# Optimization experiments

Measured on AMD Instinct MI355X. Metric: run time of the kernel, lower is better.

The kernel has to match this reference:

```python
import jax, jax.numpy as jnp
import numpy as np

N, M, D = 16384, 1024, 1024


def setup_inputs() -> dict:
    key = jax.random.key(0)
    kq, kp = jax.random.split(key)
    query = jax.random.normal(kq, (N, D), dtype=jnp.float32)
    proto = jax.random.normal(kp, (M, D), dtype=jnp.float32)
    return {"query": query, "proto": proto}


def reference(query, proto):
    # Pairwise squared euclidean: ||q||^2 - 2 q.p + ||p||^2  (same math as
    # the expand+pow+sum in compute_euclidean, but without the [N,M,D] blowup).
    q2 = jnp.sum(query * query, axis=-1, keepdims=True)          # [N,1]
    p2 = jnp.sum(proto * proto, axis=-1)                          # [M]
    qp = jnp.einsum('nd,md->nm', query, proto)                    # [N,M]
    dists = q2 - 2.0 * qp + p2[None, :]                           # [N,M]
    # Original applies F.softmax(-dists, dim=1) (named log_p_y but is softmax).
    return jax.nn.softmax(-dists, axis=1)
```

## Files before the change

### kernel.cpp

```cpp
#include <hip/hip_runtime.h>
#include <stdint.h>

#define N_Q 16384
#define M_P 1024
#define D_K 1024

typedef __attribute__((ext_vector_type(8))) __bf16 bf16x8;
typedef __attribute__((ext_vector_type(4))) float floatx4;

#define AS1 __attribute__((address_space(1)))
#define AS3 __attribute__((address_space(3)))

__device__ __forceinline__ unsigned short f2bf(float f) {
    unsigned int u = __float_as_uint(f);
    u += 0x7fffu + ((u >> 16) & 1u);
    return (unsigned short)(u >> 16);
}
__device__ __forceinline__ float bf2f(unsigned short h) {
    return __uint_as_float(((unsigned int)h) << 16);
}

__global__ __launch_bounds__(256) void convert_split_kernel(
    const float* __restrict__ src, unsigned short* __restrict__ hi,
    unsigned short* __restrict__ lo, int n4) {
    int idx = blockIdx.x * 256 + threadIdx.x;
    if (idx >= n4) return;
    float4 v = ((const float4*)src)[idx];
    float a0 = v.x, a1 = v.y, a2 = v.z, a3 = v.w;
    ushort4 h, l;
    h.x = f2bf(a0); l.x = f2bf(a0 - bf2f(h.x));
    h.y = f2bf(a1); l.y = f2bf(a1 - bf2f(h.y));
    h.z = f2bf(a2); l.z = f2bf(a2 - bf2f(h.z));
    h.w = f2bf(a3); l.w = f2bf(a3 - bf2f(h.w));
    ((ushort4*)hi)[idx] = h;
    ((ushort4*)lo)[idx] = l;
}

__global__ __launch_bounds__(256) void convert_proto_kernel(
    const float* __restrict__ proto, unsigned short* __restrict__ hi,
    unsigned short* __restrict__ lo, float* __restrict__ p2) {
    int m = blockIdx.x;
    int t = threadIdx.x;
    size_t base4 = (size_t)m * (D_K / 4) + t;
    float4 v = ((const float4*)proto)[base4];
    float a0 = v.x, a1 = v.y, a2 = v.z, a3 = v.w;
    ushort4 h, l;
    h.x = f2bf(a0); l.x = f2bf(a0 - bf2f(h.x));
    h.y = f2bf(a1); l.y = f2bf(a1 - bf2f(h.y));
    h.z = f2bf(a2); l.z = f2bf(a2 - bf2f(h.z));
    h.w = f2bf(a3); l.w = f2bf(a3 - bf2f(h.w));
    ((ushort4*)hi)[base4] = h;
    ((ushort4*)lo)[base4] = l;

    float sq = a0 * a0 + a1 * a1 + a2 * a2 + a3 * a3;
#pragma unroll
    for (int off = 1; off < 64; off <<= 1) sq += __shfl_xor(sq, off);
    __shared__ float sred[4];
    if ((t & 63) == 0) sred[t >> 6] = sq;
    __syncthreads();
    if (t == 0) p2[m] = sred[0] + sred[1] + sred[2] + sred[3];
}

__global__ __launch_bounds__(256, 3) void gemm_logits_kernel(
    const unsigned short* __restrict__ qh, const unsigned short* __restrict__ ql,
    const unsigned short* __restrict__ ph, const unsigned short* __restrict__ pl,
    const float* __restrict__ p2, float* __restrict__ out) {
    __shared__ unsigned short lds[4 * 128 * 32];

    const int tid = threadIdx.x;
    const int wave = tid >> 6;
    const int lane = tid & 63;
    const int nt = blockIdx.x & 127;
    const int mt = blockIdx.x >> 7;
    const int row0 = nt * 128;
    const int col0 = mt * 128;

    unsigned short* sAh = lds;
    unsigned short* sAl = lds + 4096;
    unsigned short* sBh = lds + 8192;
    unsigned short* sBl = lds + 12288;

    const unsigned short* gsrc;
    unsigned short* ldst;
    int grow0;
    if (wave == 0)      { gsrc = qh; grow0 = row0; ldst = sAh; }
    else if (wave == 1) { gsrc = ql; grow0 = row0; ldst = sAl; }
    else if (wave == 2) { gsrc = ph; grow0 = col0; ldst = sBh; }
    else                { gsrc = pl; grow0 = col0; ldst = sBl; }

    const int rl = lane >> 2;
    const int cio = lane & 3;
    const unsigned short* gbase = gsrc + (size_t)(grow0 + rl) * D_K + cio * 8;

    floatx4 zero = {0.0f, 0.0f, 0.0f, 0.0f};
    floatx4 acc[4][4];
#pragma unroll
    for (int i = 0; i < 4; ++i)
#pragma unroll
        for (int j = 0; j < 4; ++j) acc[i][j] = zero;

    const int wrow = (wave & 1) * 64;
    const int wcol = (wave >> 1) * 64;
    const int rsel = lane & 15;
    const int kq = lane >> 4;

    for (int kt = 0; kt < D_K / 32; ++kt) {
#pragma unroll
        for (int i = 0; i < 8; ++i) {
            const unsigned short* gp = gbase + (size_t)i * 16 * D_K + kt * 32;
            __builtin_amdgcn_global_load_lds(
                (const AS1 unsigned int*)(const void*)gp,
                (AS3 unsigned int*)(void*)(ldst + i * 512), 16, 0, 0);
        }
        __syncthreads();

        bf16x8 ah[4], al[4], bh[4], bl[4];
#pragma unroll
        for (int i = 0; i < 4; ++i) {
            const int aoff = (wrow + i * 16 + rsel) * 32 + kq * 8;
            ah[i] = *(const bf16x8*)(sAh + aoff);
            al[i] = *(const bf16x8*)(sAl + aoff);
            const int boff = (wcol + i * 16 + rsel) * 32 + kq * 8;
            bh[i] = *(const bf16x8*)(sBh + boff);
            bl[i] = *(const bf16x8*)(sBl + boff);
        }

#pragma unroll
        for (int i = 0; i < 4; ++i)
#pragma unroll
            for (int j = 0; j < 4; ++j) {
                acc[i][j] = __builtin_amdgcn_mfma_f32_16x16x32_bf16(ah[i], bh[j], acc[i][j], 0, 0, 0);
                acc[i][j] = __builtin_amdgcn_mfma_f32_16x16x32_bf16(ah[i], bl[j], acc[i][j], 0, 0, 0);
                acc[i][j] = __builtin_amdgcn_mfma_f32_16x16x32_bf16(al[i], bh[j], acc[i][j], 0, 0, 0);
            }
        __syncthreads();
    }

#pragma unroll
    for (int j = 0; j < 4; ++j) {
        const int gc = col0 + wcol + j * 16 + rsel;
        const float p2v = p2[gc];
#pragma unroll
        for (int i = 0; i < 4; ++i) {
            const int gr = row0 + wrow + i * 16 + kq * 4;
#pragma unroll
            for (int r = 0; r < 4; ++r) {
                out[(size_t)(gr + r) * M_P + gc] = 2.0f * acc[i][j][r] - p2v;
            }
        }
    }
}

__global__ __launch_bounds__(256) void naive_logits_kernel(
    const float* __restrict__ query, const float* __restrict__ proto,
    float* __restrict__ out) {
    __shared__ float qs[D_K];
    int n = blockIdx.x;
    int t = threadIdx.x;
    ((float4*)qs)[t] = ((const float4*)(query + (size_t)n * D_K))[t];
    __syncthreads();
    float acc[4] = {0.f, 0.f, 0.f, 0.f};
    float pp[4] = {0.f, 0.f, 0.f, 0.f};
    for (int d = 0; d < D_K; d += 4) {
        float4 qv = *(const float4*)(qs + d);
#pragma unroll
        for (int j = 0; j < 4; ++j) {
            const float4 pv = *(const float4*)(proto + (size_t)(t + 256 * j) * D_K + d);
            acc[j] += qv.x * pv.x + qv.y * pv.y + qv.z * pv.z + qv.w * pv.w;
            pp[j] += pv.x * pv.x + pv.y * pv.y + pv.z * pv.z + pv.w * pv.w;
        }
    }
#pragma unroll
    for (int j = 0; j < 4; ++j)
        out[(size_t)n * M_P + t + 256 * j] = 2.0f * acc[j] - pp[j];
}

__global__ __launch_bounds__(256) void softmax_kernel(float* __restrict__ out) {
    int n = blockIdx.x;
    int t = threadIdx.x;
    float4* row = (float4*)(out + (size_t)n * M_P);
    float4 v = row[t];
    float mx = fmaxf(fmaxf(v.x, v.y), fmaxf(v.z, v.w));
#pragma unroll
    for (int off = 1; off < 64; off <<= 1) mx = fmaxf(mx, __shfl_xor(mx, off));
    __shared__ float smax[4];
    __shared__ float ssum[4];
    int wave = t >> 6, lane = t & 63;
    if (lane == 0) smax[wave] = mx;
    __syncthreads();
    mx = fmaxf(fmaxf(smax[0], smax[1]), fmaxf(smax[2], smax[3]));
    float e0 = __expf(v.x - mx), e1 = __expf(v.y - mx);
    float e2 = __expf(v.z - mx), e3 = __expf(v.w - mx);
    float s = e0 + e1 + e2 + e3;
#pragma unroll
    for (int off = 1; off < 64; off <<= 1) s += __shfl_xor(s, off);
    if (lane == 0) ssum[wave] = s;
    __syncthreads();
    float inv = 1.0f / (ssum[0] + ssum[1] + ssum[2] + ssum[3]);
    float4 o;
    o.x = e0 * inv; o.y = e1 * inv; o.z = e2 * inv; o.w = e3 * inv;
    row[t] = o;
}

extern "C" void kernel_launch(void* const* d_in, const int* in_sizes, int n_in,
                              void* d_out, int out_size, void* d_ws, size_t ws_size,
                              hipStream_t stream) {
    const float* query = (const float*)d_in[0];
    const float* proto = (const float*)d_in[1];
    float* out = (float*)d_out;

    const size_t qElems = (size_t)N_Q * D_K;
    const size_t pElems = (size_t)M_P * D_K;
    const size_t needed = qElems * 2 * 2 + pElems * 2 * 2 + M_P * 4;

    if (ws_size >= needed) {
        unsigned short* qh = (unsigned short*)d_ws;
        unsigned short* ql = qh + qElems;
        unsigned short* ph = ql + qElems;
        unsigned short* pl = ph + pElems;
        float* p2 = (float*)(pl + pElems);

        convert_split_kernel<<<(int)(qElems / 4 / 256), 256, 0, stream>>>(
            query, qh, ql, (int)(qElems / 4));
        convert_proto_kernel<<<M_P, 256, 0, stream>>>(proto, ph, pl, p2);
        gemm_logits_kernel<<<(N_Q / 128) * (M_P / 128), 256, 0, stream>>>(
            qh, ql, ph, pl, p2, out);
    } else {
        naive_logits_kernel<<<N_Q, 256, 0, stream>>>(query, proto, out);
    }
    softmax_kernel<<<N_Q, 256, 0, stream>>>(out);
}
```

Measured before the change: 237.8 us.

## Remap LDS tile layout for conflict-free MFMA reads, fuse convert kernels

Changes the global-to-LDS load lane mapping so each wave's 64 lanes write exactly the fragment layout the MFMA operands need, making LDS reads contiguous and free of bank conflicts. The query and proto split conversions are merged into one launch. Nontemporal load and store hints are added for the query conversion and the softmax output. The trade-off is less coalesced global reads per row segment in the GEMM loads.

```diff
diff --git a/kernel.cpp b/kernel.cpp
--- a/kernel.cpp
+++ b/kernel.cpp
@@ -20,45 +20,42 @@
     return __uint_as_float(((unsigned int)h) << 16);
 }
 
-__global__ __launch_bounds__(256) void convert_split_kernel(
-    const float* __restrict__ src, unsigned short* __restrict__ hi,
-    unsigned short* __restrict__ lo, int n4) {
-    int idx = blockIdx.x * 256 + threadIdx.x;
-    if (idx >= n4) return;
-    float4 v = ((const float4*)src)[idx];
-    float a0 = v.x, a1 = v.y, a2 = v.z, a3 = v.w;
-    ushort4 h, l;
-    h.x = f2bf(a0); l.x = f2bf(a0 - bf2f(h.x));
-    h.y = f2bf(a1); l.y = f2bf(a1 - bf2f(h.y));
-    h.z = f2bf(a2); l.z = f2bf(a2 - bf2f(h.z));
-    h.w = f2bf(a3); l.w = f2bf(a3 - bf2f(h.w));
-    ((ushort4*)hi)[idx] = h;
-    ((ushort4*)lo)[idx] = l;
-}
-
-__global__ __launch_bounds__(256) void convert_proto_kernel(
-    const float* __restrict__ proto, unsigned short* __restrict__ hi,
-    unsigned short* __restrict__ lo, float* __restrict__ p2) {
-    int m = blockIdx.x;
+__global__ __launch_bounds__(256) void convert_all_kernel(
+    const float* __restrict__ query, unsigned short* __restrict__ qh,
+    unsigned short* __restrict__ ql, const float* __restrict__ proto,
+    unsigned short* __restrict__ ph, unsigned short* __restrict__ pl,
+    float* __restrict__ p2) {
+    __shared__ float sred[4];
+    int b = blockIdx.x;
     int t = threadIdx.x;
-    size_t base4 = (size_t)m * (D_K / 4) + t;
-    float4 v = ((const float4*)proto)[base4];
-    float a0 = v.x, a1 = v.y, a2 = v.z, a3 = v.w;
-    ushort4 h, l;
-    h.x = f2bf(a0); l.x = f2bf(a0 - bf2f(h.x));
-    h.y = f2bf(a1); l.y = f2bf(a1 - bf2f(h.y));
-    h.z = f2bf(a2); l.z = f2bf(a2 - bf2f(h.z));
-    h.w = f2bf(a3); l.w = f2bf(a3 - bf2f(h.w));
-    ((ushort4*)hi)[base4] = h;
-    ((ushort4*)lo)[base4] = l;
-
-    float sq = a0 * a0 + a1 * a1 + a2 * a2 + a3 * a3;
-#pragma unroll
-    for (int off = 1; off < 64; off <<= 1) sq += __shfl_xor(sq, off);
-    __shared__ float sred[4];
-    if ((t & 63) == 0) sred[t >> 6] = sq;
-    __syncthreads();
-    if (t == 0) p2[m] = sred[0] + sred[1] + sred[2] + sred[3];
+    if (b < N_Q) {
+        int idx = b * 256 + t;
+        floatx4 v = __builtin_nontemporal_load((const floatx4*)query + idx);
+        ushort4 h, l;
+        h.x = f2bf(v.x); l.x = f2bf(v.x - bf2f(h.x));
+        h.y = f2bf(v.y); l.y = f2bf(v.y - bf2f(h.y));
+        h.z = f2bf(v.z); l.z = f2bf(v.z - bf2f(h.z));
+        h.w = f2bf(v.w); l.w = f2bf(v.w - bf2f(h.w));
+        ((ushort4*)qh)[idx] = h;
+        ((ushort4*)ql)[idx] = l;
+    } else {
+        int m = b - N_Q;
+        size_t base4 = (size_t)m * (D_K / 4) + t;
+        float4 v = ((const float4*)proto)[base4];
+        ushort4 h, l;
+        h.x = f2bf(v.x); l.x = f2bf(v.x - bf2f(h.x));
+        h.y = f2bf(v.y); l.y = f2bf(v.y - bf2f(h.y));
+        h.z = f2bf(v.z); l.z = f2bf(v.z - bf2f(h.z));
+        h.w = f2bf(v.w); l.w = f2bf(v.w - bf2f(h.w));
+        ((ushort4*)ph)[base4] = h;
+        ((ushort4*)pl)[base4] = l;
+        float sq = v.x * v.x + v.y * v.y + v.z * v.z + v.w * v.w;
+#pragma unroll
+        for (int off = 1; off < 64; off <<= 1) sq += __shfl_xor(sq, off);
+        if ((t & 63) == 0) sred[t >> 6] = sq;
+        __syncthreads();
+        if (t == 0) p2[m] = sred[0] + sred[1] + sred[2] + sred[3];
+    }
 }
 
 __global__ __launch_bounds__(256, 3) void gemm_logits_kernel(
@@ -88,8 +85,8 @@
     else if (wave == 2) { gsrc = ph; grow0 = col0; ldst = sBh; }
     else                { gsrc = pl; grow0 = col0; ldst = sBl; }
 
-    const int rl = lane >> 2;
-    const int cio = lane & 3;
+    const int rl = lane & 15;
+    const int cio = lane >> 4;
     const unsigned short* gbase = gsrc + (size_t)(grow0 + rl) * D_K + cio * 8;
 
     floatx4 zero = {0.0f, 0.0f, 0.0f, 0.0f};
@@ -103,6 +100,8 @@
     const int wcol = (wave >> 1) * 64;
     const int rsel = lane & 15;
     const int kq = lane >> 4;
+    const int sA0 = (wrow >> 4);
+    const int sB0 = (wcol >> 4);
 
     for (int kt = 0; kt < D_K / 32; ++kt) {
 #pragma unroll
@@ -117,10 +116,10 @@
         bf16x8 ah[4], al[4], bh[4], bl[4];
 #pragma unroll
         for (int i = 0; i < 4; ++i) {
-            const int aoff = (wrow + i * 16 + rsel) * 32 + kq * 8;
+            const int aoff = (sA0 + i) * 512 + lane * 8;
             ah[i] = *(const bf16x8*)(sAh + aoff);
             al[i] = *(const bf16x8*)(sAl + aoff);
-            const int boff = (wcol + i * 16 + rsel) * 32 + kq * 8;
+            const int boff = (sB0 + i) * 512 + lane * 8;
             bh[i] = *(const bf16x8*)(sBh + boff);
             bl[i] = *(const bf16x8*)(sBl + boff);
         }
@@ -178,8 +177,8 @@
 __global__ __launch_bounds__(256) void softmax_kernel(float* __restrict__ out) {
     int n = blockIdx.x;
     int t = threadIdx.x;
-    float4* row = (float4*)(out + (size_t)n * M_P);
-    float4 v = row[t];
+    floatx4* row = (floatx4*)(out + (size_t)n * M_P);
+    floatx4 v = row[t];
     float mx = fmaxf(fmaxf(v.x, v.y), fmaxf(v.z, v.w));
 #pragma unroll
     for (int off = 1; off < 64; off <<= 1) mx = fmaxf(mx, __shfl_xor(mx, off));
@@ -197,9 +196,9 @@
     if (lane == 0) ssum[wave] = s;
     __syncthreads();
     float inv = 1.0f / (ssum[0] + ssum[1] + ssum[2] + ssum[3]);
-    float4 o;
+    floatx4 o;
     o.x = e0 * inv; o.y = e1 * inv; o.z = e2 * inv; o.w = e3 * inv;
-    row[t] = o;
+    __builtin_nontemporal_store(o, row + t);
 }
 
 extern "C" void kernel_launch(void* const* d_in, const int* in_sizes, int n_in,
@@ -220,9 +219,8 @@
         unsigned short* pl = ph + pElems;
         float* p2 = (float*)(pl + pElems);
 
-        convert_split_kernel<<<(int)(qElems / 4 / 256), 256, 0, stream>>>(
-            query, qh, ql, (int)(qElems / 4));
-        convert_proto_kernel<<<M_P, 256, 0, stream>>>(proto, ph, pl, p2);
+        convert_all_kernel<<<N_Q + M_P, 256, 0, stream>>>(
+            query, qh, ql, proto, ph, pl, p2);
         gemm_logits_kernel<<<(N_Q / 128) * (M_P / 128), 256, 0, stream>>>(
             qh, ql, ph, pl, p2, out);
     } else {
```

After: 269.4 us. +13.3%, slower.
